# Optimization experiments

Measured on AMD Instinct MI355X. Metric: run time of the kernel, lower is better.

Reference implementation:

```python
import jax, jax.numpy as jnp
import numpy as np

K = 3        # kernel_size
STRIDE = 1
PAD = 1
DIL = 1
ALPHA = 8.3


def _out_hw(n, ):
    dilated_k = K + (K - 1) * (DIL - 1)
    return (n + 2 * PAD - dilated_k + STRIDE) // STRIDE


def _patches(x, Ho, Wo):
    """im2col: x [B,C,Hp,Wp] -> [B,C,K,K,Ho,Wo] (dilated, strided windows)."""
    rows = []
    for i in range(K):
        cols = []
        for j in range(K):
            cols.append(x[:, :,
                          i * DIL: i * DIL + (Ho - 1) * STRIDE + 1: STRIDE,
                          j * DIL: j * DIL + (Wo - 1) * STRIDE + 1: STRIDE])
        rows.append(jnp.stack(cols, axis=2))          # [B,C,K,Ho,Wo]
    return jnp.stack(rows, axis=2)                    # [B,C,K,K,Ho,Wo]


def setup_inputs() -> dict:
    key = jax.random.key(0)
    k1, k2, k3, k4 = jax.random.split(key, 4)
    B, Cin, Cout, H, W = 8, 64, 64, 128, 128
    img = jax.random.normal(k1, (B, Cin, H, W), dtype=jnp.float32)
    depth = jax.random.uniform(k2, (B, 1, H, W), dtype=jnp.float32)
    weight = jax.random.normal(k3, (Cout, Cin, K, K), dtype=jnp.float32)
    bias = jax.random.normal(k4, (1, Cout), dtype=jnp.float32)
    return {"img": img, "depth": depth, "weight": weight, "bias": bias}


def reference(img, depth, weight, bias):
    B, C, H, W = img.shape
    Ho, Wo = _out_hw(H), _out_hw(W)
    pad = ((0, 0), (0, 0), (PAD, PAD), (PAD, PAD))
    img_p = jnp.pad(img, pad)
    depth_p = jnp.pad(depth, pad)

    ip = _patches(img_p, Ho, Wo)                      # [B,Cin,K,K,Ho,Wo]
    dp = _patches(depth_p, Ho, Wo)                    # [B,1,K,K,Ho,Wo]
    center = dp[:, :, K // 2: K // 2 + 1, K // 2: K // 2 + 1]  # [B,1,1,1,Ho,Wo]
    dw = jnp.exp(-ALPHA * jnp.abs(center - dp))       # depth-similarity weights

    # depth-weighted convolution: sum over Cin, K, K
    out = jnp.einsum('bcijhw,ocij->bohw', ip * dw, weight)
    return out + bias[0][None, :, None, None]
```

## Files before the change

kernel.cpp:

```cpp
#include <hip/hip_runtime.h>
#include <hip/hip_bf16.h>

#define ALPHA 8.3f
#define CIN   64
#define COUT  64
#define HH    128
#define WWD   128
#define NB    8
#define WP    130

#define WBF_BYTES (9 * COUT * CIN * 2)

typedef __attribute__((ext_vector_type(8))) short bf16x8;
typedef __attribute__((ext_vector_type(4))) float f32x4;

__device__ __forceinline__ unsigned short f2bf(float f) {
    union { float f; unsigned u; } v; v.f = f;
    unsigned u = v.u;
    return (unsigned short)((u + 0x7FFFu + ((u >> 16) & 1u)) >> 16);
}
__device__ __forceinline__ float bf2f(unsigned short s) {
    union { unsigned u; float f; } v; v.u = ((unsigned)s) << 16;
    return v.f;
}
__device__ __forceinline__ unsigned short f2bf_fast(float f) {
    union { __hip_bfloat16 h; unsigned short u; } c;
    c.h = __float2bfloat16(f);
    return c.u;
}

__device__ __forceinline__ unsigned lds_addr(int r, int wi, int c) {
    unsigned a = ((unsigned)((r * WP + wi) * CIN + c)) * 2u;
    unsigned s = ((((unsigned)wi ^ ((unsigned)wi >> 3)) & 7u) << 4);
    return a ^ s;
}

__global__ __launch_bounds__(256)
void wconv_kernel(const float* __restrict__ w, unsigned short* __restrict__ wbf) {
    int idx = blockIdx.x * 256 + threadIdx.x;
    if (idx >= 9 * COUT * CIN) return;
    int t   = idx / (COUT * CIN);
    int rem = idx - t * COUT * CIN;
    int o = rem >> 6, c = rem & 63;
    wbf[idx] = f2bf(w[(o * CIN + c) * 9 + t]);
}

__global__ __launch_bounds__(512, 4)
void conv_fused(const float* __restrict__ img,
                const float* __restrict__ depth,
                const unsigned short* __restrict__ wbf,
                const float* __restrict__ bias,
                float* __restrict__ out)
{
    __shared__ __align__(16) char smem[3 * WP * CIN * 2];

    const int b = blockIdx.x & 7;
    const int h = blockIdx.x >> 3;
    const int tid  = threadIdx.x;
    const int wv   = tid >> 6;
    const int lane = tid & 63;
    const int colq = lane & 15;
    const int kq   = lane >> 4;
    const int p0   = (wv & 3) * 32;
    const int o0   = (wv >> 2) * 32;

    const float* db = depth + (size_t)b * HH * WWD;
    float dt[2][3][3];
#pragma unroll
    for (int nt = 0; nt < 2; ++nt) {
        const int pA = p0 + nt * 16 + colq;
#pragma unroll
        for (int r = 0; r < 3; ++r) {
            int hh = h + r - 1; hh = hh < 0 ? 0 : (hh >= HH ? HH - 1 : hh);
#pragma unroll
            for (int k = 0; k < 3; ++k) {
                int pc = pA + k - 1; pc = pc < 0 ? 0 : (pc >= WWD ? WWD - 1 : pc);
                dt[nt][r][k] = db[hh * WWD + pc];
            }
        }
    }
    float bo[2];
#pragma unroll
    for (int mt = 0; mt < 2; ++mt) bo[mt] = bias[o0 + mt * 16 + colq];

    const float* ib = img + (size_t)b * CIN * HH * WWD;
#pragma unroll
    for (int it = 0; it < 12; ++it) {
        int f = tid + it * 512;
        int q = f & 31;
        int c = (f >> 5) & 63;
        int r = f >> 11;
        int hh = h + r - 1;
        float4 v = make_float4(0.f, 0.f, 0.f, 0.f);
        if (hh >= 0 && hh < HH)
            v = *(const float4*)(ib + ((size_t)c * HH + hh) * WWD + q * 4);
        const int wib = 1 + q * 4;
        *(unsigned short*)(smem + lds_addr(r, wib + 0, c)) = f2bf_fast(v.x);
        *(unsigned short*)(smem + lds_addr(r, wib + 1, c)) = f2bf_fast(v.y);
        *(unsigned short*)(smem + lds_addr(r, wib + 2, c)) = f2bf_fast(v.z);
        *(unsigned short*)(smem + lds_addr(r, wib + 3, c)) = f2bf_fast(v.w);
    }
    if (tid < 384) {
        int c = tid & 63, idx = tid >> 6;
        int r = idx >> 1, wi = (idx & 1) ? (WP - 1) : 0;
        *(unsigned short*)(smem + lds_addr(r, wi, c)) = 0;
    }
    __syncthreads();

    f32x4 acc[2][2];
#pragma unroll
    for (int nt = 0; nt < 2; ++nt)
#pragma unroll
        for (int mt = 0; mt < 2; ++mt)
            acc[nt][mt] = (f32x4){bo[mt], bo[mt], bo[mt], bo[mt]};

#pragma unroll
    for (int i = 0; i < 3; ++i) {
        bf16x8 Bf[3][2][2];
#pragma unroll
        for (int j = 0; j < 3; ++j)
#pragma unroll
            for (int kst = 0; kst < 2; ++kst)
#pragma unroll
                for (int mt = 0; mt < 2; ++mt)
                    Bf[j][kst][mt] = *(const bf16x8*)(wbf
                        + (i * 3 + j) * (COUT * CIN)
                        + (o0 + mt * 16 + colq) * CIN + kst * 32 + kq * 8);

#pragma unroll
        for (int j = 0; j < 3; ++j) {
#pragma unroll
            for (int nt = 0; nt < 2; ++nt) {
                const float dw = __expf(-ALPHA * fabsf(dt[nt][1][1] - dt[nt][i][j]));
                const int wi = p0 + nt * 16 + colq + j;
#pragma unroll
                for (int kst = 0; kst < 2; ++kst) {
                    bf16x8 A = *(const bf16x8*)(smem + lds_addr(i, wi, kst * 32 + kq * 8));
                    union { bf16x8 v; unsigned short u[8]; } ain, as;
                    ain.v = A;
#pragma unroll
                    for (int e = 0; e < 8; ++e)
                        as.u[e] = f2bf_fast(bf2f(ain.u[e]) * dw);
#pragma unroll
                    for (int mt = 0; mt < 2; ++mt)
                        acc[nt][mt] = __builtin_amdgcn_mfma_f32_16x16x32_bf16(
                                          as.v, Bf[j][kst][mt], acc[nt][mt], 0, 0, 0);
                }
            }
        }
    }

#pragma unroll
    for (int mt = 0; mt < 2; ++mt) {
        const int o = o0 + mt * 16 + colq;
#pragma unroll
        for (int nt = 0; nt < 2; ++nt)
            *(f32x4*)(out + (((size_t)b * COUT + o) * HH + h) * WWD
                          + p0 + nt * 16 + kq * 4) = acc[nt][mt];
    }
}

__global__ __launch_bounds__(128)
void depthconv_fallback(const float* __restrict__ img, const float* __restrict__ depth,
                        const float* __restrict__ weight, const float* __restrict__ bias,
                        float* __restrict__ out)
{
    const int bh = blockIdx.x;
    const int b  = bh >> 7;
    const int h  = bh & (HH - 1);
    const int w  = threadIdx.x;

    const float* dbase = depth + (size_t)b * HH * WWD;
    const float  dc    = dbase[h * WWD + w];

    float dwm[9]; int off[9];
#pragma unroll
    for (int i = 0; i < 3; ++i) {
        const int  hh2 = h + i - 1;
        const bool hok = (hh2 >= 0) && (hh2 < HH);
        const int  hc  = hok ? hh2 : h;
#pragma unroll
        for (int j = 0; j < 3; ++j) {
            const int  ww  = w + j - 1;
            const bool wok = (ww >= 0) && (ww < WWD);
            const int  wc  = wok ? ww : w;
            const bool ok  = hok && wok;
            const float dv = ok ? dbase[hh2 * WWD + ww] : 0.f;
            dwm[i * 3 + j] = (ok ? 1.f : 0.f) * __expf(-ALPHA * fabsf(dc - dv));
            off[i * 3 + j] = hc * WWD + wc;
        }
    }
    float acc[COUT];
#pragma unroll
    for (int o = 0; o < COUT; ++o) acc[o] = 0.f;
    const float* ibase = img + (size_t)b * CIN * HH * WWD;
#pragma unroll 1
    for (int c = 0; c < CIN; ++c) {
        float v[9];
#pragma unroll
        for (int t = 0; t < 9; ++t) v[t] = ibase[(size_t)c * HH * WWD + off[t]] * dwm[t];
        const float* wc_ = weight + c * 9;
#pragma unroll
        for (int o = 0; o < COUT; ++o) {
            const float* wp = wc_ + o * (CIN * 9);
#pragma unroll
            for (int t = 0; t < 9; ++t) acc[o] = fmaf(v[t], wp[t], acc[o]);
        }
    }
#pragma unroll
    for (int o = 0; o < COUT; ++o)
        out[(((size_t)b * COUT + o) * HH + h) * WWD + w] = acc[o] + bias[o];
}

extern "C" void kernel_launch(void* const* d_in, const int* in_sizes, int n_in,
                              void* d_out, int out_size, void* d_ws, size_t ws_size,
                              hipStream_t stream)
{
    const float* img    = (const float*)d_in[0];
    const float* depth  = (const float*)d_in[1];
    const float* weight = (const float*)d_in[2];
    const float* bias   = (const float*)d_in[3];
    float*       out    = (float*)d_out;

    if (ws_size >= (size_t)WBF_BYTES) {
        unsigned short* wbf = (unsigned short*)d_ws;
        wconv_kernel<<<(9 * COUT * CIN + 255) / 256, 256, 0, stream>>>(weight, wbf);
        conv_fused<<<NB * HH, 512, 0, stream>>>(img, depth, wbf, bias, out);
    } else {
        depthconv_fallback<<<NB * HH, WWD, 0, stream>>>(img, depth, weight, bias, out);
    }
}
```

Before: 125.8 us.

## Apply depth weights to MFMA outputs instead of scaling bf16 inputs per tap

The depth weight depends only on the output pixel and tap, not on the channel, so it can be factored out of the channel sum. Each wave now runs a plain MFMA of unweighted LDS activations against the weights into a per-tap temporary, then scales the result by the per-pixel depth weight with fp32 FMAs. The centre tap has weight 1 and accumulates directly. This removes the per-element bf16 unpack/multiply/repack from the inner loop, at the cost of more accumulator registers, a change of wave tiling to 16 pixels by 64 outputs, a simpler LDS swizzle and a lower occupancy bound.

```diff
diff --git a/kernel.cpp b/kernel.cpp
--- a/kernel.cpp
+++ b/kernel.cpp
@@ -19,10 +19,6 @@
     unsigned u = v.u;
     return (unsigned short)((u + 0x7FFFu + ((u >> 16) & 1u)) >> 16);
 }
-__device__ __forceinline__ float bf2f(unsigned short s) {
-    union { unsigned u; float f; } v; v.u = ((unsigned)s) << 16;
-    return v.f;
-}
 __device__ __forceinline__ unsigned short f2bf_fast(float f) {
     union { __hip_bfloat16 h; unsigned short u; } c;
     c.h = __float2bfloat16(f);
@@ -31,8 +27,7 @@
 
 __device__ __forceinline__ unsigned lds_addr(int r, int wi, int c) {
     unsigned a = ((unsigned)((r * WP + wi) * CIN + c)) * 2u;
-    unsigned s = ((((unsigned)wi ^ ((unsigned)wi >> 3)) & 7u) << 4);
-    return a ^ s;
+    return a ^ (((unsigned)wi & 7u) << 4);
 }
 
 __global__ __launch_bounds__(256)
@@ -45,12 +40,12 @@
     wbf[idx] = f2bf(w[(o * CIN + c) * 9 + t]);
 }
 
-__global__ __launch_bounds__(512, 4)
-void conv_fused(const float* __restrict__ img,
-                const float* __restrict__ depth,
-                const unsigned short* __restrict__ wbf,
-                const float* __restrict__ bias,
-                float* __restrict__ out)
+__global__ __launch_bounds__(512, 2)
+void conv_fused4(const float* __restrict__ img,
+                 const float* __restrict__ depth,
+                 const unsigned short* __restrict__ wbf,
+                 const float* __restrict__ bias,
+                 float* __restrict__ out)
 {
     __shared__ __align__(16) char smem[3 * WP * CIN * 2];
 
@@ -61,27 +56,7 @@
     const int lane = tid & 63;
     const int colq = lane & 15;
     const int kq   = lane >> 4;
-    const int p0   = (wv & 3) * 32;
-    const int o0   = (wv >> 2) * 32;
-
-    const float* db = depth + (size_t)b * HH * WWD;
-    float dt[2][3][3];
-#pragma unroll
-    for (int nt = 0; nt < 2; ++nt) {
-        const int pA = p0 + nt * 16 + colq;
-#pragma unroll
-        for (int r = 0; r < 3; ++r) {
-            int hh = h + r - 1; hh = hh < 0 ? 0 : (hh >= HH ? HH - 1 : hh);
-#pragma unroll
-            for (int k = 0; k < 3; ++k) {
-                int pc = pA + k - 1; pc = pc < 0 ? 0 : (pc >= WWD ? WWD - 1 : pc);
-                dt[nt][r][k] = db[hh * WWD + pc];
-            }
-        }
-    }
-    float bo[2];
-#pragma unroll
-    for (int mt = 0; mt < 2; ++mt) bo[mt] = bias[o0 + mt * 16 + colq];
+    const int p0   = wv * 16;
 
     const float* ib = img + (size_t)b * CIN * HH * WWD;
 #pragma unroll
@@ -105,59 +80,81 @@
         int r = idx >> 1, wi = (idx & 1) ? (WP - 1) : 0;
         *(unsigned short*)(smem + lds_addr(r, wi, c)) = 0;
     }
+
+    const float* db = depth + (size_t)b * HH * WWD;
+    const int pb = p0 + kq * 4;
+    float dt[3][6];
+#pragma unroll
+    for (int r2 = 0; r2 < 3; ++r2) {
+        int hh = h + r2 - 1; hh = hh < 0 ? 0 : (hh >= HH ? HH - 1 : hh);
+#pragma unroll
+        for (int k = 0; k < 6; ++k) {
+            int pc = pb - 1 + k; pc = pc < 0 ? 0 : (pc >= WWD ? WWD - 1 : pc);
+            dt[r2][k] = db[hh * WWD + pc];
+        }
+    }
+    float dw8[8][4];
+#pragma unroll
+    for (int i = 0; i < 3; ++i)
+#pragma unroll
+        for (int j = 0; j < 3; ++j) {
+            if (i == 1 && j == 1) continue;
+            const int t  = i * 3 + j;
+            const int ti = t < 4 ? t : t - 1;
+#pragma unroll
+            for (int rr = 0; rr < 4; ++rr)
+                dw8[ti][rr] = __expf(-ALPHA * fabsf(dt[1][1 + rr] - dt[i][rr + j]));
+        }
+    float bo[4];
+#pragma unroll
+    for (int mt = 0; mt < 4; ++mt) bo[mt] = bias[mt * 16 + colq];
+
     __syncthreads();
 
-    f32x4 acc[2][2];
-#pragma unroll
-    for (int nt = 0; nt < 2; ++nt)
-#pragma unroll
-        for (int mt = 0; mt < 2; ++mt)
-            acc[nt][mt] = (f32x4){bo[mt], bo[mt], bo[mt], bo[mt]};
+    f32x4 acc[4];
+#pragma unroll
+    for (int mt = 0; mt < 4; ++mt) acc[mt] = (f32x4){bo[mt], bo[mt], bo[mt], bo[mt]};
 
 #pragma unroll
     for (int i = 0; i < 3; ++i) {
-        bf16x8 Bf[3][2][2];
-#pragma unroll
-        for (int j = 0; j < 3; ++j)
-#pragma unroll
-            for (int kst = 0; kst < 2; ++kst)
-#pragma unroll
-                for (int mt = 0; mt < 2; ++mt)
-                    Bf[j][kst][mt] = *(const bf16x8*)(wbf
-                        + (i * 3 + j) * (COUT * CIN)
-                        + (o0 + mt * 16 + colq) * CIN + kst * 32 + kq * 8);
-
 #pragma unroll
         for (int j = 0; j < 3; ++j) {
-#pragma unroll
-            for (int nt = 0; nt < 2; ++nt) {
-                const float dw = __expf(-ALPHA * fabsf(dt[nt][1][1] - dt[nt][i][j]));
-                const int wi = p0 + nt * 16 + colq + j;
-#pragma unroll
-                for (int kst = 0; kst < 2; ++kst) {
-                    bf16x8 A = *(const bf16x8*)(smem + lds_addr(i, wi, kst * 32 + kq * 8));
-                    union { bf16x8 v; unsigned short u[8]; } ain, as;
-                    ain.v = A;
-#pragma unroll
-                    for (int e = 0; e < 8; ++e)
-                        as.u[e] = f2bf_fast(bf2f(ain.u[e]) * dw);
-#pragma unroll
-                    for (int mt = 0; mt < 2; ++mt)
-                        acc[nt][mt] = __builtin_amdgcn_mfma_f32_16x16x32_bf16(
-                                          as.v, Bf[j][kst][mt], acc[nt][mt], 0, 0, 0);
+            const unsigned short* wt = wbf + (i * 3 + j) * (COUT * CIN);
+            const bf16x8 A0 = *(const bf16x8*)(smem + lds_addr(i, p0 + colq + j, kq * 8));
+            const bf16x8 A1 = *(const bf16x8*)(smem + lds_addr(i, p0 + colq + j, 32 + kq * 8));
+            if (i == 1 && j == 1) {
+#pragma unroll
+                for (int mt = 0; mt < 4; ++mt) {
+                    const bf16x8 B0 = *(const bf16x8*)(wt + (mt * 16 + colq) * CIN + kq * 8);
+                    const bf16x8 B1 = *(const bf16x8*)(wt + (mt * 16 + colq) * CIN + 32 + kq * 8);
+                    acc[mt] = __builtin_amdgcn_mfma_f32_16x16x32_bf16(A0, B0, acc[mt], 0, 0, 0);
+                    acc[mt] = __builtin_amdgcn_mfma_f32_16x16x32_bf16(A1, B1, acc[mt], 0, 0, 0);
                 }
+            } else {
+                const int ti = (i * 3 + j) < 4 ? (i * 3 + j) : (i * 3 + j) - 1;
+                f32x4 conv[4];
+#pragma unroll
+                for (int mt = 0; mt < 4; ++mt) conv[mt] = (f32x4){0.f, 0.f, 0.f, 0.f};
+#pragma unroll
+                for (int mt = 0; mt < 4; ++mt) {
+                    const bf16x8 B0 = *(const bf16x8*)(wt + (mt * 16 + colq) * CIN + kq * 8);
+                    const bf16x8 B1 = *(const bf16x8*)(wt + (mt * 16 + colq) * CIN + 32 + kq * 8);
+                    conv[mt] = __builtin_amdgcn_mfma_f32_16x16x32_bf16(A0, B0, conv[mt], 0, 0, 0);
+                    conv[mt] = __builtin_amdgcn_mfma_f32_16x16x32_bf16(A1, B1, conv[mt], 0, 0, 0);
+                }
+#pragma unroll
+                for (int mt = 0; mt < 4; ++mt)
+#pragma unroll
+                    for (int rr = 0; rr < 4; ++rr)
+                        acc[mt][rr] = fmaf(dw8[ti][rr], conv[mt][rr], acc[mt][rr]);
             }
         }
     }
 
 #pragma unroll
-    for (int mt = 0; mt < 2; ++mt) {
-        const int o = o0 + mt * 16 + colq;
-#pragma unroll
-        for (int nt = 0; nt < 2; ++nt)
-            *(f32x4*)(out + (((size_t)b * COUT + o) * HH + h) * WWD
-                          + p0 + nt * 16 + kq * 4) = acc[nt][mt];
-    }
+    for (int mt = 0; mt < 4; ++mt)
+        *(f32x4*)(out + (((size_t)b * COUT + mt * 16 + colq) * HH + h) * WWD
+                      + p0 + kq * 4) = acc[mt];
 }
 
 __global__ __launch_bounds__(128)
@@ -225,7 +222,7 @@
     if (ws_size >= (size_t)WBF_BYTES) {
         unsigned short* wbf = (unsigned short*)d_ws;
         wconv_kernel<<<(9 * COUT * CIN + 255) / 256, 256, 0, stream>>>(weight, wbf);
-        conv_fused<<<NB * HH, 512, 0, stream>>>(img, depth, wbf, bias, out);
+        conv_fused4<<<NB * HH, 512, 0, stream>>>(img, depth, wbf, bias, out);
     } else {
         depthconv_fallback<<<NB * HH, WWD, 0, stream>>>(img, depth, weight, bias, out);
     }
```

New measurement: 172.1 us. 1.37x slower.
